# Performance work log

Hardware: AMD Instinct MI355X
Metric: run time of the kernel (lower is better)

## Reference

```python
import jax, jax.numpy as jnp
import numpy as np

N_HEADS = 16

def setup_inputs() -> dict:
    key = jax.random.key(0)
    k1, k2 = jax.random.split(key)
    qkv = jax.random.normal(k1, (4, 3072, 2048), dtype=jnp.float32)
    encoder_kv = jax.random.normal(k2, (4, 2048, 256), dtype=jnp.float32)
    return {"qkv": qkv, "encoder_kv": encoder_kv}

def reference(qkv, encoder_kv):
    bs, width, length = qkv.shape
    ch = width // (3 * N_HEADS)  # 64
    # [bs*H, 3*ch, T] -> q, k, v each [bs*H, ch, T]
    q, k, v = jnp.split(qkv.reshape(bs * N_HEADS, 3 * ch, length), 3, axis=1)
    # encoder kv: [bs, H*2*ch, S] -> ek, ev each [bs*H, ch, S]
    ek, ev = jnp.split(encoder_kv.reshape(bs * N_HEADS, 2 * ch, -1), 2, axis=1)
    k = jnp.concatenate([ek, k], axis=-1)  # [bs*H, ch, S+T]
    v = jnp.concatenate([ev, v], axis=-1)
    scale = ch ** -0.25  # 1/sqrt(sqrt(ch)), applied to both q and k
    weight = jnp.einsum('bct,bcs->bts', q * scale, k * scale)  # [bs*H, T, S+T]
    weight = jax.nn.softmax(weight.astype(jnp.float32), axis=-1).astype(qkv.dtype)
    a = jnp.einsum('bts,bcs->bct', weight, v)  # [bs*H, ch, T]
    return a.reshape(bs, -1, length)
```

## Files before the change

kernel.cpp:

```cpp
#include <hip/hip_runtime.h>
#include <hip/hip_bf16.h>

typedef __attribute__((ext_vector_type(8))) short bf16x8;
typedef __attribute__((ext_vector_type(8))) short s16x8;
typedef __attribute__((ext_vector_type(4))) short s16x4;
typedef __attribute__((ext_vector_type(4))) float f32x4;

#define T_LEN 2048
#define S_ENC 256
#define ROW 72
#define QSCALE 0.18033688011112042f

#if __has_builtin(__builtin_amdgcn_exp2f)
#define EXP2(x) __builtin_amdgcn_exp2f(x)
#else
#define EXP2(x) exp2f(x)
#endif

__device__ __forceinline__ short f2bf(float x) {
  union { __hip_bfloat16 b; short s; } u;
  u.b = __float2bfloat16(x);
  return u.s;
}

template<int STRIDE>
__device__ __forceinline__ void tile_body(
    const float* __restrict__ kb, const float* __restrict__ vb, int s0,
    short* __restrict__ Kt, short* __restrict__ Vt,
    const bf16x8 (&qf)[2][2], f32x4 (&o)[2][4], float (&lp)[2], int tid) {

  const int lane = tid & 63;
  const int ln = lane & 15;
  const int lg = lane >> 4;

  const int ks = tid & 63;
  const int kc = (tid >> 6) * 8;
  float kr[8];
  const float* kp = kb + (size_t)kc * STRIDE + (s0 + ks);
#pragma unroll
  for (int r = 0; r < 8; ++r) kr[r] = kp[(size_t)r * STRIDE];

  const int vg = tid & 15;
  const int vc = tid >> 4;
  const int vcol = 32 * (vg >> 3) + 8 * (vg & 3) + 4 * ((vg >> 2) & 1);
  const float* vp0 = vb + (size_t)vc * STRIDE + (s0 + 4 * vg);
  f32x4 vr0 = *(const f32x4*)(vp0);
  f32x4 vr1 = *(const f32x4*)(vp0 + (size_t)32 * STRIDE);

  __syncthreads();

  s16x8 kw;
#pragma unroll
  for (int r = 0; r < 8; ++r) kw[r] = f2bf(kr[r]);
  *(s16x8*)(Kt + ks * ROW + kc) = kw;

  s16x4 vw;
#pragma unroll
  for (int i = 0; i < 4; ++i) vw[i] = f2bf(vr0[i]);
  *(s16x4*)(Vt + vc * ROW + vcol) = vw;
#pragma unroll
  for (int i = 0; i < 4; ++i) vw[i] = f2bf(vr1[i]);
  *(s16x4*)(Vt + (vc + 32) * ROW + vcol) = vw;

  __syncthreads();

  f32x4 sacc[2][4];
#pragma unroll
  for (int qt = 0; qt < 2; ++qt)
#pragma unroll
    for (int mt = 0; mt < 4; ++mt) sacc[qt][mt] = (f32x4){0.f, 0.f, 0.f, 0.f};

#pragma unroll
  for (int mt = 0; mt < 4; ++mt) {
    const short* krow = Kt + (16 * mt + ln) * ROW + 8 * lg;
    const bf16x8 kf0 = *(const bf16x8*)(krow);
    const bf16x8 kf1 = *(const bf16x8*)(krow + 32);
#pragma unroll
    for (int qt = 0; qt < 2; ++qt) {
      sacc[qt][mt] = __builtin_amdgcn_mfma_f32_16x16x32_bf16(kf0, qf[qt][0], sacc[qt][mt], 0, 0, 0);
      sacc[qt][mt] = __builtin_amdgcn_mfma_f32_16x16x32_bf16(kf1, qf[qt][1], sacc[qt][mt], 0, 0, 0);
    }
  }

  bf16x8 pfrag[2][2];
#pragma unroll
  for (int qt = 0; qt < 2; ++qt) {
    float ls = 0.f;
#pragma unroll
    for (int mt = 0; mt < 4; ++mt)
#pragma unroll
      for (int r = 0; r < 4; ++r) {
        const float p = EXP2(sacc[qt][mt][r]);
        ls += p;
        pfrag[qt][mt >> 1][4 * (mt & 1) + r] = f2bf(p);
      }
    lp[qt] += ls;
  }

#pragma unroll
  for (int sub = 0; sub < 2; ++sub)
#pragma unroll
    for (int ct = 0; ct < 4; ++ct) {
      const bf16x8 vf = *(const bf16x8*)(Vt + (16 * ct + ln) * ROW + 32 * sub + 8 * lg);
#pragma unroll
      for (int qt = 0; qt < 2; ++qt)
        o[qt][ct] = __builtin_amdgcn_mfma_f32_16x16x32_bf16(vf, pfrag[qt][sub], o[qt][ct], 0, 0, 0);
    }
}

__global__ __launch_bounds__(512, 4) void attn_kernel(
    const float* __restrict__ qkv, const float* __restrict__ ekv,
    float* __restrict__ out) {
  const int tid = threadIdx.x;
  const int lane = tid & 63;
  const int wave = tid >> 6;
  const int ln = lane & 15;
  const int lg = lane >> 4;

  const int bh = blockIdx.x >> 3;
  const int qb = blockIdx.x & 7;
  const int t0 = qb * 256 + wave * 32;

  const float* qp  = qkv + (size_t)bh * 192 * T_LEN;
  const float* kp  = qp + (size_t)64 * T_LEN;
  const float* vp  = qp + (size_t)128 * T_LEN;
  const float* ekp = ekv + (size_t)bh * 128 * S_ENC;
  const float* evp = ekp + (size_t)64 * S_ENC;

  __shared__ __attribute__((aligned(16))) short Kt[64 * ROW];
  __shared__ __attribute__((aligned(16))) short Vt[64 * ROW];

  bf16x8 qf[2][2];
#pragma unroll
  for (int qt = 0; qt < 2; ++qt)
#pragma unroll
    for (int kk = 0; kk < 2; ++kk)
#pragma unroll
      for (int j = 0; j < 8; ++j)
        qf[qt][kk][j] =
            f2bf(qp[(size_t)(32 * kk + 8 * lg + j) * T_LEN + (t0 + 16 * qt + ln)] * QSCALE);

  f32x4 o[2][4];
#pragma unroll
  for (int qt = 0; qt < 2; ++qt)
#pragma unroll
    for (int ct = 0; ct < 4; ++ct) o[qt][ct] = (f32x4){0.f, 0.f, 0.f, 0.f};
  float lp[2] = {0.f, 0.f};

  for (int st = 0; st < 4; ++st)
    tile_body<S_ENC>(ekp, evp, 64 * st, Kt, Vt, qf, o, lp, tid);
  for (int st = 0; st < 32; ++st)
    tile_body<T_LEN>(kp, vp, 64 * st, Kt, Vt, qf, o, lp, tid);

#pragma unroll
  for (int qt = 0; qt < 2; ++qt) {
    float l = lp[qt];
    l += __shfl_xor(l, 16);
    l += __shfl_xor(l, 32);
    const float inv = 1.0f / l;
    float* ob = out + (size_t)bh * 64 * T_LEN + (t0 + 16 * qt + ln);
#pragma unroll
    for (int ct = 0; ct < 4; ++ct)
#pragma unroll
      for (int r = 0; r < 4; ++r)
        ob[(size_t)(16 * ct + 4 * lg + r) * T_LEN] = o[qt][ct][r] * inv;
  }
}

extern "C" void kernel_launch(void* const* d_in, const int* in_sizes, int n_in,
                              void* d_out, int out_size, void* d_ws, size_t ws_size,
                              hipStream_t stream) {
  const float* qkv = (const float*)d_in[0];
  const float* ekv = (const float*)d_in[1];
  float* out = (float*)d_out;
  attn_kernel<<<dim3(512), dim3(512), 0, stream>>>(qkv, ekv, out);
}
```

Measured before the change: 109.2 us.

## Swizzle LDS tiles, use lighter barriers, tree-sum exponentials, remap block order

Replaces the padded 72-short LDS rows with a 64-wide XOR-swizzled layout to avoid bank conflicts and shrink shared memory. Replaces __syncthreads with an explicit lgkmcnt wait plus s_barrier. Also restructures the softmax row sum into a tree, switches EXP2 from the amdgcn builtin to exp2f, and reorders blockIdx so consecutive blocks cover different heads. The exp2f change may add range-handling instructions, and the head-major block order changes L2 locality for K/V reuse.

```diff
diff --git a/kernel.cpp b/kernel.cpp
--- a/kernel.cpp
+++ b/kernel.cpp
@@ -8,19 +8,23 @@
 
 #define T_LEN 2048
 #define S_ENC 256
-#define ROW 72
 #define QSCALE 0.18033688011112042f
+#define EXP2(x) exp2f(x)
 
-#if __has_builtin(__builtin_amdgcn_exp2f)
-#define EXP2(x) __builtin_amdgcn_exp2f(x)
-#else
-#define EXP2(x) exp2f(x)
-#endif
+#define BARRIER()                                         \
+  do {                                                    \
+    asm volatile("s_waitcnt lgkmcnt(0)" ::: "memory");    \
+    __builtin_amdgcn_s_barrier();                         \
+  } while (0)
 
 __device__ __forceinline__ short f2bf(float x) {
   union { __hip_bfloat16 b; short s; } u;
   u.b = __float2bfloat16(x);
   return u.s;
+}
+
+__device__ __forceinline__ int swz(int row, int col) {
+  return row * 64 + (col ^ ((row & 7) << 3));
 }
 
 template<int STRIDE>
@@ -42,27 +46,27 @@
 
   const int vg = tid & 15;
   const int vc = tid >> 4;
-  const int vcol = 32 * (vg >> 3) + 8 * (vg & 3) + 4 * ((vg >> 2) & 1);
   const float* vp0 = vb + (size_t)vc * STRIDE + (s0 + 4 * vg);
   f32x4 vr0 = *(const f32x4*)(vp0);
   f32x4 vr1 = *(const f32x4*)(vp0 + (size_t)32 * STRIDE);
 
-  __syncthreads();
+  BARRIER();
 
   s16x8 kw;
 #pragma unroll
   for (int r = 0; r < 8; ++r) kw[r] = f2bf(kr[r]);
-  *(s16x8*)(Kt + ks * ROW + kc) = kw;
+  *(s16x8*)(Kt + swz(ks, kc)) = kw;
 
+  const int vcol = 32 * (vg >> 3) + 8 * (vg & 3) + 4 * ((vg >> 2) & 1);
   s16x4 vw;
 #pragma unroll
   for (int i = 0; i < 4; ++i) vw[i] = f2bf(vr0[i]);
-  *(s16x4*)(Vt + vc * ROW + vcol) = vw;
+  *(s16x4*)(Vt + swz(vc, vcol)) = vw;
 #pragma unroll
   for (int i = 0; i < 4; ++i) vw[i] = f2bf(vr1[i]);
-  *(s16x4*)(Vt + (vc + 32) * ROW + vcol) = vw;
+  *(s16x4*)(Vt + swz(vc + 32, vcol)) = vw;
 
-  __syncthreads();
+  BARRIER();
 
   f32x4 sacc[2][4];
 #pragma unroll
@@ -72,9 +76,9 @@
 
 #pragma unroll
   for (int mt = 0; mt < 4; ++mt) {
-    const short* krow = Kt + (16 * mt + ln) * ROW + 8 * lg;
-    const bf16x8 kf0 = *(const bf16x8*)(krow);
-    const bf16x8 kf1 = *(const bf16x8*)(krow + 32);
+    const int row = 16 * mt + ln;
+    const bf16x8 kf0 = *(const bf16x8*)(Kt + swz(row, 8 * lg));
+    const bf16x8 kf1 = *(const bf16x8*)(Kt + swz(row, 32 + 8 * lg));
 #pragma unroll
     for (int qt = 0; qt < 2; ++qt) {
       sacc[qt][mt] = __builtin_amdgcn_mfma_f32_16x16x32_bf16(kf0, qf[qt][0], sacc[qt][mt], 0, 0, 0);
@@ -85,23 +89,27 @@
   bf16x8 pfrag[2][2];
 #pragma unroll
   for (int qt = 0; qt < 2; ++qt) {
-    float ls = 0.f;
+    float pmt[4];
 #pragma unroll
-    for (int mt = 0; mt < 4; ++mt)
-#pragma unroll
-      for (int r = 0; r < 4; ++r) {
-        const float p = EXP2(sacc[qt][mt][r]);
-        ls += p;
-        pfrag[qt][mt >> 1][4 * (mt & 1) + r] = f2bf(p);
-      }
-    lp[qt] += ls;
+    for (int mt = 0; mt < 4; ++mt) {
+      float p0 = EXP2(sacc[qt][mt][0]);
+      float p1 = EXP2(sacc[qt][mt][1]);
+      float p2 = EXP2(sacc[qt][mt][2]);
+      float p3 = EXP2(sacc[qt][mt][3]);
+      pfrag[qt][mt >> 1][4 * (mt & 1) + 0] = f2bf(p0);
+      pfrag[qt][mt >> 1][4 * (mt & 1) + 1] = f2bf(p1);
+      pfrag[qt][mt >> 1][4 * (mt & 1) + 2] = f2bf(p2);
+      pfrag[qt][mt >> 1][4 * (mt & 1) + 3] = f2bf(p3);
+      pmt[mt] = (p0 + p1) + (p2 + p3);
+    }
+    lp[qt] += (pmt[0] + pmt[1]) + (pmt[2] + pmt[3]);
   }
 
 #pragma unroll
   for (int sub = 0; sub < 2; ++sub)
 #pragma unroll
     for (int ct = 0; ct < 4; ++ct) {
-      const bf16x8 vf = *(const bf16x8*)(Vt + (16 * ct + ln) * ROW + 32 * sub + 8 * lg);
+      const bf16x8 vf = *(const bf16x8*)(Vt + swz(16 * ct + ln, 32 * sub + 8 * lg));
 #pragma unroll
       for (int qt = 0; qt < 2; ++qt)
         o[qt][ct] = __builtin_amdgcn_mfma_f32_16x16x32_bf16(vf, pfrag[qt][sub], o[qt][ct], 0, 0, 0);
@@ -117,8 +125,8 @@
   const int ln = lane & 15;
   const int lg = lane >> 4;
 
-  const int bh = blockIdx.x >> 3;
-  const int qb = blockIdx.x & 7;
+  const int bh = blockIdx.x & 63;
+  const int qb = blockIdx.x >> 6;
   const int t0 = qb * 256 + wave * 32;
 
   const float* qp  = qkv + (size_t)bh * 192 * T_LEN;
@@ -127,8 +135,8 @@
   const float* ekp = ekv + (size_t)bh * 128 * S_ENC;
   const float* evp = ekp + (size_t)64 * S_ENC;
 
-  __shared__ __attribute__((aligned(16))) short Kt[64 * ROW];
-  __shared__ __attribute__((aligned(16))) short Vt[64 * ROW];
+  __shared__ __attribute__((aligned(16))) short Kt[64 * 64];
+  __shared__ __attribute__((aligned(16))) short Vt[64 * 64];
 
   bf16x8 qf[2][2];
 #pragma unroll
```

New measurement: 123.4 us. 13.1% more time.
